# Optimization experiments

Hardware: AMD Instinct MI355X
Metric: run time of the kernel (lower is better)

## Reference

```python
import jax, jax.numpy as jnp
import numpy as np

B, S, D, H = 2, 2048, 1024, 16
HD = D // H  # head_dim = 64
SCALE = HD ** -0.5


def setup_inputs() -> dict:
    key = jax.random.key(0)
    ks = jax.random.split(key, 10)
    std = D ** -0.5
    return {
        "x": jax.random.normal(ks[0], (B, S, D), jnp.float32),
        "y": jax.random.normal(ks[1], (B, S, D), jnp.float32),
        "Wq": jax.random.normal(ks[2], (D, D), jnp.float32) * std,
        "bq": jnp.zeros((D,), jnp.float32),
        "Wk": jax.random.normal(ks[3], (D, D), jnp.float32) * std,
        "bk": jnp.zeros((D,), jnp.float32),
        "Wv": jax.random.normal(ks[4], (D, D), jnp.float32) * std,
        "bv": jnp.zeros((D,), jnp.float32),
        "Wo": jax.random.normal(ks[5], (D, D), jnp.float32) * std,
        "bo": jnp.zeros((D,), jnp.float32),
    }


def reference(x, y, Wq, bq, Wk, bk, Wv, bv, Wo, bo):
    # Linear projections (torch Linear: x @ W.T + b; here W stored as [in,out])
    q = x @ Wq + bq  # [B,S,D]
    k = y @ Wk + bk
    v = y @ Wv + bv
    # split heads -> [B,H,S,hd]
    q = q.reshape(B, S, H, HD).transpose(0, 2, 1, 3)
    k = k.reshape(B, S, H, HD).transpose(0, 2, 1, 3)
    v = v.reshape(B, S, H, HD).transpose(0, 2, 1, 3)
    scores = jnp.einsum("bhqd,bhkd->bhqk", q, k) * SCALE  # [B,H,S,S]
    causal = jnp.tril(jnp.ones((S, S), dtype=bool))  # keep lower triangle
    scores = jnp.where(causal[None, None], scores, -jnp.inf)
    attn = jax.nn.softmax(scores, axis=-1)
    out = jnp.einsum("bhqk,bhkd->bhqd", attn, v)  # [B,H,S,hd]
    out = out.transpose(0, 2, 1, 3).reshape(B, S, D)
    return out @ Wo + bo
```

## Files before the change

kernel.cpp:

```cpp
#include <hip/hip_runtime.h>
#include <hip/hip_bf16.h>


#define BDIM 2
#define SDIM 2048
#define DDIM 1024
#define HDIM 16
#define HD   64
#define MDIM (BDIM*SDIM)
#define C2 0.18033688011112042f

using short8  = __attribute__((ext_vector_type(8))) short;
using floatx4 = __attribute__((ext_vector_type(4))) float;

static __device__ __forceinline__ unsigned short f2bf(float x) {
    union { float f; unsigned int u; } c; c.f = x;
    unsigned int r = (c.u + 0x7fffu + ((c.u >> 16) & 1u)) >> 16;
    return (unsigned short)r;
}

static __device__ __forceinline__ unsigned int pack2bf(float a, float b) {
    union { float f; unsigned int u; } ua, ub;
    ua.f = a; ub.f = b;
    return __builtin_amdgcn_perm(ub.u + 0x8000u, ua.u + 0x8000u, 0x07060302u);
}

#define GLD16(g, l) __builtin_amdgcn_global_load_lds(                        \
    (const __attribute__((address_space(1))) void*)(g),                      \
    (__attribute__((address_space(3))) void*)(l), 16, 0, 0)

__global__ __launch_bounds__(256) void prep_kernel(
    const float* __restrict__ X, const float* __restrict__ Y,
    const float* __restrict__ W0, const float* __restrict__ W1,
    const float* __restrict__ W2, const float* __restrict__ W3,
    unsigned short* __restrict__ Xo, unsigned short* __restrict__ Yo,
    unsigned short* __restrict__ T0, unsigned short* __restrict__ T1,
    unsigned short* __restrict__ T2, unsigned short* __restrict__ T3)
{
    __shared__ float tile[64][68];
    const int z = blockIdx.z;
    const int t = threadIdx.x;
    if (z < 2) {
        const float* A    = z ? Y : X;
        unsigned short* O = z ? Yo : Xo;
        const int idx = blockIdx.x * 256 + t;
        const float4 a = ((const float4*)A)[idx*2];
        const float4 b = ((const float4*)A)[idx*2 + 1];
        ushort4 lo, hi;
        lo.x = f2bf(a.x); lo.y = f2bf(a.y); lo.z = f2bf(a.z); lo.w = f2bf(a.w);
        hi.x = f2bf(b.x); hi.y = f2bf(b.y); hi.z = f2bf(b.z); hi.w = f2bf(b.w);
        ((ushort4*)O)[idx*2]     = lo;
        ((ushort4*)O)[idx*2 + 1] = hi;
        return;
    }
    if (blockIdx.x >= 256) return;
    const int zz = z - 2;
    const float* W    = (zz == 0) ? W0 : (zz == 1) ? W1 : (zz == 2) ? W2 : W3;
    unsigned short* T = (zz == 0) ? T0 : (zz == 1) ? T1 : (zz == 2) ? T2 : T3;
    const int k0 = (blockIdx.x & 15) * 64, n0 = (blockIdx.x >> 4) * 64;
    #pragma unroll
    for (int i = 0; i < 4; ++i) {
        const int idx = t + i*256;
        const int kr = idx >> 4, c4 = idx & 15;
        float4 v = *(const float4*)&W[(size_t)(k0 + kr) * DDIM + n0 + c4*4];
        tile[kr][c4*4+0] = v.x; tile[kr][c4*4+1] = v.y;
        tile[kr][c4*4+2] = v.z; tile[kr][c4*4+3] = v.w;
    }
    __syncthreads();
    #pragma unroll
    for (int i = 0; i < 4; ++i) {
        const int idx = t + i*256;
        const int nr = idx >> 4, kc = idx & 15;
        ushort4 o;
        o.x = f2bf(tile[kc*4+0][nr]); o.y = f2bf(tile[kc*4+1][nr]);
        o.z = f2bf(tile[kc*4+2][nr]); o.w = f2bf(tile[kc*4+3][nr]);
        *(ushort4*)&T[(size_t)(n0 + nr) * DDIM + k0 + kc*4] = o;
    }
}

template <bool SWAP>
__device__ __forceinline__ void gemm128_core(
    const unsigned short* __restrict__ A, const unsigned short* __restrict__ Bt,
    int bm, int bn, unsigned short* As, unsigned short* Bs, floatx4 acc[4][4])
{
    const int t = threadIdx.x;
    const int w = t >> 6, l = t & 63;
    const int quad = l >> 4, col = l & 15;
    const int wr = (w >> 1) * 64, wc = (w & 1) * 64;

    const int c1 = t + 256;
    const int r0 = t >> 2,  o0 = (t & 3) * 8;
    const int r1 = c1 >> 2, o1 = (c1 & 3) * 8;

    const unsigned short* Ar0 = A  + (size_t)(bm + r0) * DDIM + o0;
    const unsigned short* Ar1 = A  + (size_t)(bm + r1) * DDIM + o1;
    const unsigned short* Br0 = Bt + (size_t)(bn + r0) * DDIM + o0;
    const unsigned short* Br1 = Bt + (size_t)(bn + r1) * DDIM + o1;

    GLD16(Ar0, As + t*8);
    GLD16(Ar1, As + c1*8);
    GLD16(Br0, Bs + t*8);
    GLD16(Br1, Bs + c1*8);

    for (int kt = 0; kt < DDIM; kt += 32) {
        const int cur = (kt >> 5) & 1;
        unsigned short* Asn = As + (cur ^ 1) * 4096;
        unsigned short* Bsn = Bs + (cur ^ 1) * 4096;
        __syncthreads();
        if (kt + 32 < DDIM) {
            GLD16(Ar0 + kt + 32, Asn + t*8);
            GLD16(Ar1 + kt + 32, Asn + c1*8);
            GLD16(Br0 + kt + 32, Bsn + t*8);
            GLD16(Br1 + kt + 32, Bsn + c1*8);
        }
        const unsigned short* Asc = As + cur*4096;
        const unsigned short* Bsc = Bs + cur*4096;
        short8 af[4], bfr[4];
        #pragma unroll
        for (int i = 0; i < 4; ++i)
            af[i] = *(const short8*)&Asc[(wr + i*16 + col)*32 + quad*8];
        #pragma unroll
        for (int j = 0; j < 4; ++j)
            bfr[j] = *(const short8*)&Bsc[(wc + j*16 + col)*32 + quad*8];
        #pragma unroll
        for (int i = 0; i < 4; ++i)
            #pragma unroll
            for (int j = 0; j < 4; ++j)
                acc[i][j] = SWAP
                    ? __builtin_amdgcn_mfma_f32_16x16x32_bf16(bfr[j], af[i], acc[i][j], 0, 0, 0)
                    : __builtin_amdgcn_mfma_f32_16x16x32_bf16(af[i], bfr[j], acc[i][j], 0, 0, 0);
    }
}

__global__ __launch_bounds__(256) void qkv_gemm_kernel(
    const unsigned short* __restrict__ xbf, const unsigned short* __restrict__ ybf,
    const unsigned short* __restrict__ Wqt, const unsigned short* __restrict__ Wkt,
    const unsigned short* __restrict__ Wvt,
    const float* __restrict__ bq, const float* __restrict__ bk,
    const float* __restrict__ bv,
    unsigned short* __restrict__ Qbf, unsigned short* __restrict__ Kbf,
    unsigned short* __restrict__ vT)
{
    __shared__ __align__(16) unsigned short As[2*4096];
    __shared__ __align__(16) unsigned short Bs[2*4096];

    const int z = blockIdx.z;
    const unsigned short* A  = (z == 0) ? xbf : ybf;
    const unsigned short* Wt = (z == 0) ? Wqt : (z == 1) ? Wkt : Wvt;
    const float* bp          = (z == 0) ? bq  : (z == 1) ? bk  : bv;

    const int bm = (blockIdx.x * 4 + (blockIdx.y & 3)) * 128;
    const int bn = (blockIdx.y >> 2) * 128;

    const int t = threadIdx.x;
    const int w = t >> 6, l = t & 63;
    const int quad = l >> 4, col = l & 15;
    const int wr = (w >> 1) * 64, wc = (w & 1) * 64;

    floatx4 acc[4][4] = {};

    if (z < 2) {
        gemm128_core<true>(A, Wt, bm, bn, As, Bs, acc);
        unsigned short* O = (z == 0) ? Qbf : Kbf;
        const float sc = (z == 0) ? C2 : 1.0f;
        float4 bias4[4];
        #pragma unroll
        for (int j = 0; j < 4; ++j)
            bias4[j] = *(const float4*)&bp[bn + wc + j*16 + quad*4];
        #pragma unroll
        for (int i = 0; i < 4; ++i) {
            const int m = bm + wr + i*16 + col;
            unsigned short* rowp = O + (size_t)m * DDIM;
            #pragma unroll
            for (int j = 0; j < 4; ++j) {
                const float v0 = (acc[i][j][0] + bias4[j].x) * sc;
                const float v1 = (acc[i][j][1] + bias4[j].y) * sc;
                const float v2 = (acc[i][j][2] + bias4[j].z) * sc;
                const float v3 = (acc[i][j][3] + bias4[j].w) * sc;
                uint2 pk;
                pk.x = pack2bf(v0, v1);
                pk.y = pack2bf(v2, v3);
                *(uint2*)&rowp[bn + wc + j*16 + quad*4] = pk;
            }
        }
    } else {
        gemm128_core<false>(A, Wt, bm, bn, As, Bs, acc);
        #pragma unroll
        for (int j = 0; j < 4; ++j) {
            const int gn = bn + wc + j*16 + col;
            const float bias = bp[gn];
            #pragma unroll
            for (int i = 0; i < 4; ++i) {
                const int gm0 = bm + wr + i*16 + quad*4;
                uint2 pk;
                pk.x = pack2bf(acc[i][j][0] + bias, acc[i][j][1] + bias);
                pk.y = pack2bf(acc[i][j][2] + bias, acc[i][j][3] + bias);
                *(uint2*)&vT[((size_t)((gm0 >> 11) * DDIM + gn)) * SDIM + (gm0 & 2047)] = pk;
            }
        }
    }
}

__global__ __launch_bounds__(256) void out_gemm_kernel(
    const unsigned short* __restrict__ Obf, const unsigned short* __restrict__ Wot,
    const float* __restrict__ bo, float* __restrict__ out)
{
    __shared__ __align__(16) unsigned short As[2*4096];
    __shared__ __align__(16) unsigned short Bs[2*2048];

    const int t = threadIdx.x;
    const int w = t >> 6, l = t & 63;
    const int quad = l >> 4, col = l & 15;

    const int j  = (blockIdx.x >> 3) + 2 * blockIdx.y;
    const int bm = ((blockIdx.x & 7) * 4 + (j & 3)) * 128;
    const int bn = (j >> 2) * 64;

    const int wr = (w >> 1) * 64, wc = (w & 1) * 32;

    const int r0 = t >> 2, o0 = (t & 3) * 8;
    const unsigned short* Ar0 = Obf + (size_t)(bm + r0) * DDIM + o0;
    const unsigned short* Ar1 = Obf + (size_t)(bm + 64 + r0) * DDIM + o0;
    const unsigned short* Br  = Wot + (size_t)(bn + r0) * DDIM + o0;

    floatx4 acc[4][2] = {};

    GLD16(Ar0, As + t*8);
    GLD16(Ar1, As + (t + 256)*8);
    GLD16(Br,  Bs + t*8);

    for (int kt = 0; kt < DDIM; kt += 32) {
        const int cur = (kt >> 5) & 1;
        unsigned short* Asn = As + (cur ^ 1) * 4096;
        unsigned short* Bsn = Bs + (cur ^ 1) * 2048;
        __syncthreads();
        if (kt + 32 < DDIM) {
            GLD16(Ar0 + kt + 32, Asn + t*8);
            GLD16(Ar1 + kt + 32, Asn + (t + 256)*8);
            GLD16(Br  + kt + 32, Bsn + t*8);
        }
        const unsigned short* Asc = As + cur*4096;
        const unsigned short* Bsc = Bs + cur*2048;
        short8 af[4], bfr[2];
        #pragma unroll
        for (int i = 0; i < 4; ++i)
            af[i] = *(const short8*)&Asc[(wr + i*16 + col)*32 + quad*8];
        #pragma unroll
        for (int j2 = 0; j2 < 2; ++j2)
            bfr[j2] = *(const short8*)&Bsc[(wc + j2*16 + col)*32 + quad*8];
        #pragma unroll
        for (int i = 0; i < 4; ++i)
            #pragma unroll
            for (int j2 = 0; j2 < 2; ++j2)
                acc[i][j2] = __builtin_amdgcn_mfma_f32_16x16x32_bf16(
                    bfr[j2], af[i], acc[i][j2], 0, 0, 0);
    }

    float4 bias4[2];
    #pragma unroll
    for (int j2 = 0; j2 < 2; ++j2)
        bias4[j2] = *(const float4*)&bo[bn + wc + j2*16 + quad*4];
    #pragma unroll
    for (int i = 0; i < 4; ++i) {
        const int m = bm + wr + i*16 + col;
        float* rowp = out + (size_t)m * DDIM;
        #pragma unroll
        for (int j2 = 0; j2 < 2; ++j2) {
            float4 o;
            o.x = acc[i][j2][0] + bias4[j2].x;
            o.y = acc[i][j2][1] + bias4[j2].y;
            o.z = acc[i][j2][2] + bias4[j2].z;
            o.w = acc[i][j2][3] + bias4[j2].w;
            *(float4*)&rowp[bn + wc + j2*16 + quad*4] = o;
        }
    }
}

__global__ __launch_bounds__(256, 2) void attn_mfma_kernel(
    const unsigned short* __restrict__ Qbf, const unsigned short* __restrict__ Kbf,
    const unsigned short* __restrict__ vT, unsigned short* __restrict__ Obf)
{
    __shared__ float ls[2][4*64];
    __shared__ __align__(16) floatx4 os[2][1024];

    const int t = threadIdx.x;
    const int w = t >> 6, l = t & 63;
    const int quad = l >> 4, col = l & 15;

    const int lin = blockIdx.x;
    const int jj  = lin >> 3, rem = jj & 3;
    const int p   = jj >> 2;
    const int b   = rem & 1;
    const int h   = (lin & 7) + 8 * (rem >> 1);

    const size_t hoff = (size_t)h * HD;
    const size_t bS   = (size_t)b * SDIM;
    const size_t bD   = (size_t)b * DDIM;

    const int rowp = ((col >> 2) << 3) | (col & 3);
    const unsigned short* kb0 = Kbf + bS * DDIM + hoff + quad*8;
    const unsigned short* vb0 = vT + (bD + hoff + col) * SDIM + quad*8;

    #pragma unroll 1
    for (int ph = 0; ph < 2; ++ph) {
        const int qT = ph ? p : (31 - p);
        const int qb = qT * 64;

        short8 qf[4][2];
        #pragma unroll
        for (int m = 0; m < 4; ++m)
            #pragma unroll
            for (int hf = 0; hf < 2; ++hf)
                qf[m][hf] = *(const short8*)
                    &Qbf[(bS + qb + m*16 + col) * DDIM + hoff + hf*32 + quad*8];

        floatx4 o[4][4] = {};
        float lrun[4] = {0.f, 0.f, 0.f, 0.f};

        #pragma unroll 1
        for (int it = w; it <= qT; it += 4) {
            const int ktb = it * 64;
            const bool diag = (it == qT);

            short8 kf[2][2][2];
            #pragma unroll
            for (int c = 0; c < 2; ++c)
                #pragma unroll
                for (int tt = 0; tt < 2; ++tt) {
                    const size_t row = (size_t)(ktb + c*32 + tt*4 + rowp);
                    kf[c][tt][0] = *(const short8*)&kb0[row * DDIM];
                    kf[c][tt][1] = *(const short8*)&kb0[row * DDIM + 32];
                }
            short8 vf[4][2];
            #pragma unroll
            for (int n = 0; n < 4; ++n)
                #pragma unroll
                for (int c = 0; c < 2; ++c)
                    vf[n][c] = *(const short8*)
                        &vb0[(size_t)(n*16) * SDIM + ktb + c*32];

            #pragma unroll
            for (int m = 0; m < 4; ++m) {
                #pragma unroll
                for (int c = 0; c < 2; ++c) {
                    if (diag && (c*32 > m*16 + 15)) continue;
                    const bool needm = diag && (c*32 + 31 > m*16);

                    floatx4 s0 = {}, s1 = {};
                    __builtin_amdgcn_s_setprio(1);
                    s0 = __builtin_amdgcn_mfma_f32_16x16x32_bf16(kf[c][0][0], qf[m][0], s0, 0, 0, 0);
                    s0 = __builtin_amdgcn_mfma_f32_16x16x32_bf16(kf[c][0][1], qf[m][1], s0, 0, 0, 0);
                    s1 = __builtin_amdgcn_mfma_f32_16x16x32_bf16(kf[c][1][0], qf[m][0], s1, 0, 0, 0);
                    s1 = __builtin_amdgcn_mfma_f32_16x16x32_bf16(kf[c][1][1], qf[m][1], s1, 0, 0, 0);
                    __builtin_amdgcn_s_setprio(0);

                    float p0[4], p1[4];
                    const int qrow = m*16 + col;
                    const int kls  = c*32 + quad*8;
                    #pragma unroll
                    for (int rr = 0; rr < 4; ++rr) {
                        p0[rr] = (needm && (kls + rr     > qrow)) ? 0.0f : exp2f(s0[rr]);
                        p1[rr] = (needm && (kls + 4 + rr > qrow)) ? 0.0f : exp2f(s1[rr]);
                    }
                    lrun[m] += ((p0[0]+p0[1]) + (p0[2]+p0[3]))
                             + ((p1[0]+p1[1]) + (p1[2]+p1[3]));

                    union { short8 v; unsigned int u[4]; } pf;
                    pf.u[0] = pack2bf(p0[0], p0[1]);
                    pf.u[1] = pack2bf(p0[2], p0[3]);
                    pf.u[2] = pack2bf(p1[0], p1[1]);
                    pf.u[3] = pack2bf(p1[2], p1[3]);

                    __builtin_amdgcn_s_setprio(1);
                    #pragma unroll
                    for (int n = 0; n < 4; ++n)
                        o[n][m] = __builtin_amdgcn_mfma_f32_16x16x32_bf16(
                            vf[n][c], pf.v, o[n][m], 0, 0, 0);
                    __builtin_amdgcn_s_setprio(0);
                }
            }
        }

        if (w >= 2) {
            const int s = w - 2;
            #pragma unroll
            for (int n = 0; n < 4; ++n)
                #pragma unroll
                for (int m = 0; m < 4; ++m)
                    os[s][(n*4 + m)*64 + l] = o[n][m];
            #pragma unroll
            for (int m = 0; m < 4; ++m)
                ls[s][m*64 + l] = lrun[m];
        }
        __syncthreads();
        if (w < 2) {
            #pragma unroll
            for (int n = 0; n < 4; ++n)
                #pragma unroll
                for (int m = 0; m < 4; ++m)
                    o[n][m] += os[w][(n*4 + m)*64 + l];
            #pragma unroll
            for (int m = 0; m < 4; ++m)
                lrun[m] += ls[w][m*64 + l];
        }
        __syncthreads();
        if (w == 1) {
            #pragma unroll
            for (int n = 0; n < 4; ++n)
                #pragma unroll
                for (int m = 0; m < 4; ++m)
                    os[0][(n*4 + m)*64 + l] = o[n][m];
            #pragma unroll
            for (int m = 0; m < 4; ++m)
                ls[0][m*64 + l] = lrun[m];
        }
        __syncthreads();
        if (w == 0) {
            #pragma unroll
            for (int m = 0; m < 4; ++m) {
                float lt = lrun[m] + ls[0][m*64 + l];
                lt += __shfl_xor(lt, 16);
                lt += __shfl_xor(lt, 32);
                const float inv = 1.0f / lt;
                #pragma unroll
                for (int n = 0; n < 4; ++n) {
                    const floatx4 ov = o[n][m] + os[0][(n*4 + m)*64 + l];
                    uint2 pk;
                    pk.x = pack2bf(ov[0] * inv, ov[1] * inv);
                    pk.y = pack2bf(ov[2] * inv, ov[3] * inv);
                    *(uint2*)&Obf[(bS + qb + m*16 + col) * DDIM
                                  + hoff + n*16 + quad*4] = pk;
                }
            }
        }
        __syncthreads();
    }
}

extern "C" void kernel_launch(void* const* d_in, const int* in_sizes, int n_in,
                              void* d_out, int out_size, void* d_ws, size_t ws_size,
                              hipStream_t stream) {
    const float* x  = (const float*)d_in[0];
    const float* y  = (const float*)d_in[1];
    const float* Wq = (const float*)d_in[2];
    const float* bq = (const float*)d_in[3];
    const float* Wk = (const float*)d_in[4];
    const float* bk = (const float*)d_in[5];
    const float* Wv = (const float*)d_in[6];
    const float* bv = (const float*)d_in[7];
    const float* Wo = (const float*)d_in[8];
    const float* bo = (const float*)d_in[9];
    float* out = (float*)d_out;

    const size_t mat  = (size_t)MDIM * DDIM;
    const size_t wmat = (size_t)DDIM * DDIM;
    unsigned short* p = (unsigned short*)d_ws;
    unsigned short* xbf = p;            p += mat;
    unsigned short* ybf = p;            p += mat;
    unsigned short* Wqt = p;            p += wmat;
    unsigned short* Wkt = p;            p += wmat;
    unsigned short* Wvt = p;            p += wmat;
    unsigned short* Wot = p;            p += wmat;
    unsigned short* Qbf = p;            p += mat;
    unsigned short* Kbf = p;            p += mat;
    unsigned short* vT  = p;            p += mat;
    unsigned short* Obf = p;            p += mat;

    hipLaunchKernelGGL(prep_kernel, dim3(MDIM*DDIM/8/256, 1, 6), dim3(256),
                       0, stream, x, y, Wq, Wk, Wv, Wo,
                       xbf, ybf, Wqt, Wkt, Wvt, Wot);

    hipLaunchKernelGGL(qkv_gemm_kernel, dim3(DDIM/128, MDIM/128, 3), dim3(256),
                       0, stream, xbf, ybf, Wqt, Wkt, Wvt, bq, bk, bv,
                       Qbf, Kbf, vT);

    hipLaunchKernelGGL(attn_mfma_kernel, dim3(512), dim3(256),
                       0, stream, Qbf, Kbf, vT, Obf);

    hipLaunchKernelGGL(out_gemm_kernel, dim3(DDIM/64, MDIM/128), dim3(256),
                       0, stream, Obf, Wot, bo, out);
}
```

Measured before the change: 207.8 us.

## Use six waves per attention block and merge weight-transpose grid planes

The attention kernel now runs 384 threads (6 waves) per block, striding key tiles by 6 instead of 4, and uses a three-slot shared-memory reduction to combine partial outputs and row sums. The K/V fragment loads move inside the per-chunk loop to reduce register pressure so the kernel fits launch bounds of 3 blocks per CU. The prep kernel packs the four weight transposes into a single z-plane (blockIdx.x selects the matrix), cutting the grid from 6 to 3 z-planes and removing many early-exit blocks. The risks are a more serialized cross-wave reduction with extra barriers and possible register spilling under the tighter bound.

```diff
diff --git a/kernel.cpp b/kernel.cpp
--- a/kernel.cpp
+++ b/kernel.cpp
@@ -53,11 +53,12 @@
         ((ushort4*)O)[idx*2 + 1] = hi;
         return;
     }
-    if (blockIdx.x >= 256) return;
-    const int zz = z - 2;
+    if (blockIdx.x >= 1024) return;
+    const int zz = blockIdx.x >> 8;
+    const int tx = blockIdx.x & 255;
     const float* W    = (zz == 0) ? W0 : (zz == 1) ? W1 : (zz == 2) ? W2 : W3;
     unsigned short* T = (zz == 0) ? T0 : (zz == 1) ? T1 : (zz == 2) ? T2 : T3;
-    const int k0 = (blockIdx.x & 15) * 64, n0 = (blockIdx.x >> 4) * 64;
+    const int k0 = (tx & 15) * 64, n0 = (tx >> 4) * 64;
     #pragma unroll
     for (int i = 0; i < 4; ++i) {
         const int idx = t + i*256;
@@ -276,12 +277,12 @@
     }
 }
 
-__global__ __launch_bounds__(256, 2) void attn_mfma_kernel(
+__global__ __launch_bounds__(384, 3) void attn_mfma_kernel(
     const unsigned short* __restrict__ Qbf, const unsigned short* __restrict__ Kbf,
     const unsigned short* __restrict__ vT, unsigned short* __restrict__ Obf)
 {
-    __shared__ float ls[2][4*64];
-    __shared__ __align__(16) floatx4 os[2][1024];
+    __shared__ __align__(16) floatx4 os[3][1024];
+    __shared__ float ls[3][256];
 
     const int t = threadIdx.x;
     const int w = t >> 6, l = t & 63;
@@ -318,40 +319,36 @@
         float lrun[4] = {0.f, 0.f, 0.f, 0.f};
 
         #pragma unroll 1
-        for (int it = w; it <= qT; it += 4) {
+        for (int it = w; it <= qT; it += 6) {
             const int ktb = it * 64;
             const bool diag = (it == qT);
 
-            short8 kf[2][2][2];
-            #pragma unroll
-            for (int c = 0; c < 2; ++c)
+            #pragma unroll
+            for (int c = 0; c < 2; ++c) {
+                short8 kfc[2][2];
                 #pragma unroll
                 for (int tt = 0; tt < 2; ++tt) {
                     const size_t row = (size_t)(ktb + c*32 + tt*4 + rowp);
-                    kf[c][tt][0] = *(const short8*)&kb0[row * DDIM];
-                    kf[c][tt][1] = *(const short8*)&kb0[row * DDIM + 32];
+                    kfc[tt][0] = *(const short8*)&kb0[row * DDIM];
+                    kfc[tt][1] = *(const short8*)&kb0[row * DDIM + 32];
                 }
-            short8 vf[4][2];
-            #pragma unroll
-            for (int n = 0; n < 4; ++n)
-                #pragma unroll
-                for (int c = 0; c < 2; ++c)
-                    vf[n][c] = *(const short8*)
+                short8 vfc[4];
+                #pragma unroll
+                for (int n = 0; n < 4; ++n)
+                    vfc[n] = *(const short8*)
                         &vb0[(size_t)(n*16) * SDIM + ktb + c*32];
 
-            #pragma unroll
-            for (int m = 0; m < 4; ++m) {
-                #pragma unroll
-                for (int c = 0; c < 2; ++c) {
+                #pragma unroll
+                for (int m = 0; m < 4; ++m) {
                     if (diag && (c*32 > m*16 + 15)) continue;
                     const bool needm = diag && (c*32 + 31 > m*16);
 
                     floatx4 s0 = {}, s1 = {};
                     __builtin_amdgcn_s_setprio(1);
-                    s0 = __builtin_amdgcn_mfma_f32_16x16x32_bf16(kf[c][0][0], qf[m][0], s0, 0, 0, 0);
-                    s0 = __builtin_amdgcn_mfma_f32_16x16x32_bf16(kf[c][0][1], qf[m][1], s0, 0, 0, 0);
-                    s1 = __builtin_amdgcn_mfma_f32_16x16x32_bf16(kf[c][1][0], qf[m][0], s1, 0, 0, 0);
-                    s1 = __builtin_amdgcn_mfma_f32_16x16x32_bf16(kf[c][1][1], qf[m][1], s1, 0, 0, 0);
+                    s0 = __builtin_amdgcn_mfma_f32_16x16x32_bf16(kfc[0][0], qf[m][0], s0, 0, 0, 0);
+                    s0 = __builtin_amdgcn_mfma_f32_16x16x32_bf16(kfc[0][1], qf[m][1], s0, 0, 0, 0);
+                    s1 = __builtin_amdgcn_mfma_f32_16x16x32_bf16(kfc[1][0], qf[m][0], s1, 0, 0, 0);
+                    s1 = __builtin_amdgcn_mfma_f32_16x16x32_bf16(kfc[1][1], qf[m][1], s1, 0, 0, 0);
                     __builtin_amdgcn_s_setprio(0);
 
                     float p0[4], p1[4];
@@ -375,14 +372,14 @@
                     #pragma unroll
                     for (int n = 0; n < 4; ++n)
                         o[n][m] = __builtin_amdgcn_mfma_f32_16x16x32_bf16(
-                            vf[n][c], pf.v, o[n][m], 0, 0, 0);
+                            vfc[n], pf.v, o[n][m], 0, 0, 0);
                     __builtin_amdgcn_s_setprio(0);
                 }
             }
         }
 
-        if (w >= 2) {
-            const int s = w - 2;
+        if (w >= 3) {
+            const int s = w - 3;
             #pragma unroll
             for (int n = 0; n < 4; ++n)
                 #pragma unroll
@@ -393,7 +390,7 @@
                 ls[s][m*64 + l] = lrun[m];
         }
         __syncthreads();
-        if (w < 2) {
+        if (w < 3) {
             #pragma unroll
             for (int n = 0; n < 4; ++n)
                 #pragma unroll
@@ -404,27 +401,29 @@
                 lrun[m] += ls[w][m*64 + l];
         }
         __syncthreads();
-        if (w == 1) {
+        if (w == 1 || w == 2) {
+            const int s = w - 1;
             #pragma unroll
             for (int n = 0; n < 4; ++n)
                 #pragma unroll
                 for (int m = 0; m < 4; ++m)
-                    os[0][(n*4 + m)*64 + l] = o[n][m];
+                    os[s][(n*4 + m)*64 + l] = o[n][m];
             #pragma unroll
             for (int m = 0; m < 4; ++m)
-                ls[0][m*64 + l] = lrun[m];
+                ls[s][m*64 + l] = lrun[m];
         }
         __syncthreads();
         if (w == 0) {
             #pragma unroll
             for (int m = 0; m < 4; ++m) {
-                float lt = lrun[m] + ls[0][m*64 + l];
+                float lt = lrun[m] + ls[0][m*64 + l] + ls[1][m*64 + l];
                 lt += __shfl_xor(lt, 16);
                 lt += __shfl_xor(lt, 32);
                 const float inv = 1.0f / lt;
                 #pragma unroll
                 for (int n = 0; n < 4; ++n) {
-                    const floatx4 ov = o[n][m] + os[0][(n*4 + m)*64 + l];
+                    const floatx4 ov = o[n][m] + os[0][(n*4 + m)*64 + l]
+                                               + os[1][(n*4 + m)*64 + l];
                     uint2 pk;
                     pk.x = pack2bf(ov[0] * inv, ov[1] * inv);
                     pk.y = pack2bf(ov[2] * inv, ov[3] * inv);
@@ -466,7 +465,7 @@
     unsigned short* vT  = p;            p += mat;
     unsigned short* Obf = p;            p += mat;
 
-    hipLaunchKernelGGL(prep_kernel, dim3(MDIM*DDIM/8/256, 1, 6), dim3(256),
+    hipLaunchKernelGGL(prep_kernel, dim3(MDIM*DDIM/8/256, 1, 3), dim3(256),
                        0, stream, x, y, Wq, Wk, Wv, Wo,
                        xbf, ybf, Wqt, Wkt, Wvt, Wot);
 
@@ -474,7 +473,7 @@
                        0, stream, xbf, ybf, Wqt, Wkt, Wvt, bq, bk, bv,
                        Qbf, Kbf, vT);
 
-    hipLaunchKernelGGL(attn_mfma_kernel, dim3(512), dim3(256),
+    hipLaunchKernelGGL(attn_mfma_kernel, dim3(512), dim3(384),
                        0, stream, Qbf, Kbf, vT, Obf);
 
     hipLaunchKernelGGL(out_gemm_kernel, dim3(DDIM/64, MDIM/128), dim3(256),
```

Result: slower. 241.5 us (+16.2%).
